# Performance work log

Measured on AMD Instinct MI355X. Metric: run time of the kernel, lower is better.

Reference implementation:

```python
import jax, jax.numpy as jnp
import numpy as np

N = 50000
E = 800000
D_IN = 128
D_OUT = 128


def setup_inputs() -> dict:
    key = jax.random.key(0)
    ks = jax.random.split(key, 12)
    x = jax.random.normal(ks[0], (N, D_IN), dtype=jnp.float32)
    W1 = jax.random.normal(ks[1], (D_IN, D_OUT), dtype=jnp.float32) * (1.0 / np.sqrt(D_IN))
    b1 = jnp.zeros((D_OUT,), dtype=jnp.float32)
    W2 = jax.random.normal(ks[2], (D_IN, D_OUT), dtype=jnp.float32) * (1.0 / np.sqrt(D_IN))
    b2 = jnp.zeros((D_OUT,), dtype=jnp.float32)
    # inverted-dropout masks, p=0.5 -> values in {0, 2}
    def mask(k):
        return jnp.where(jax.random.uniform(k, (N, D_IN)) < 0.5, 0.0, 2.0).astype(jnp.float32)
    mask_pos1 = mask(ks[3])
    mask_neg1 = mask(ks[4])
    mask_pos2 = mask(ks[5])
    mask_neg2 = mask(ks[6])
    edge_index1 = jax.random.randint(ks[7], (2, E), 0, N, dtype=jnp.int32)
    edge_index2 = jax.random.randint(ks[8], (2, E), 0, N, dtype=jnp.int32)
    perm1 = jax.random.permutation(ks[9], N).astype(jnp.int32)
    perm2 = jax.random.permutation(ks[10], N).astype(jnp.int32)
    return dict(x=x, W1=W1, b1=b1, W2=W2, b2=b2,
                mask_pos1=mask_pos1, mask_neg1=mask_neg1,
                mask_pos2=mask_pos2, mask_neg2=mask_neg2,
                edge_index1=edge_index1, edge_index2=edge_index2,
                perm1=perm1, perm2=perm2)


def gcn_conv(x, W, b, edge_index):
    """PyG GCNConv: add self-loops, symmetric normalization, then x@W aggregation + bias."""
    n = x.shape[0]
    xw = x @ W  # [N, D_OUT]
    loops = jnp.arange(n, dtype=edge_index.dtype)
    src = jnp.concatenate([edge_index[0], loops])
    dst = jnp.concatenate([edge_index[1], loops])
    deg = jax.ops.segment_sum(jnp.ones_like(dst, dtype=xw.dtype), dst, num_segments=n)
    dinv = jax.lax.rsqrt(jnp.maximum(deg, 1.0))  # deg >= 1 due to self-loops
    norm = dinv[src] * dinv[dst]                 # [E+N]
    msg = xw[src] * norm[:, None]                # [E+N, D_OUT]
    out = jax.ops.segment_sum(msg, dst, num_segments=n)
    return out + b


def _branch(x, W, b, edge_index, mask_pos, mask_neg, perm):
    pos_h = jax.nn.relu(gcn_conv(x * mask_pos, W, b, edge_index))
    neg_in = (x * mask_neg)[perm]
    neg_h = jax.nn.relu(gcn_conv(neg_in, W, b, edge_index))
    summary = jnp.mean(pos_h, axis=0, keepdims=True)  # [1, D_OUT]
    return pos_h, neg_h, summary


def reference(x, W1, b1, W2, b2, mask_pos1, mask_neg1, mask_pos2, mask_neg2,
              edge_index1, edge_index2, perm1, perm2):
    p1, n1, s1 = _branch(x, W1, b1, edge_index1, mask_pos1, mask_neg1, perm1)
    p2, n2, s2 = _branch(x, W2, b2, edge_index2, mask_pos2, mask_neg2, perm2)
    return (p1, n1, s1, p2, n2, s2)
```

## Files before the change

kernel.cpp:

```cpp
#include <hip/hip_runtime.h>
#include <hip/hip_fp16.h>

#define NN 50000
#define NE 800000
#define D 128
#define GEMM_BLOCKS 3128
#define NBKT 64
#define BW 782
#define BCAP 16384

typedef _Float16 half8_t __attribute__((ext_vector_type(8)));
typedef _Float16 half4_t __attribute__((ext_vector_type(4)));
typedef float f32x4 __attribute__((ext_vector_type(4)));

__global__ void k_init(float* s1, float* s2, int* bcnt,
                       const float* __restrict__ W1, const float* __restrict__ W2,
                       _Float16* wt1, _Float16* wt2) {
    int i = blockIdx.x * 256 + threadIdx.x;
    if (i < D) { s1[i] = 0.f; s2[i] = 0.f; }
    if (i < 2 * NBKT) bcnt[i] = 0;
    int n = i >> 7, k = i & 127;
    wt1[n * 128 + k] = (_Float16)W1[k * 128 + n];
    wt2[n * 128 + k] = (_Float16)W2[k * 128 + n];
}

__global__ void k_bucket(const int* __restrict__ src1, const int* __restrict__ dst1,
                         const int* __restrict__ src2, const int* __restrict__ dst2,
                         int* bcnt,
                         int* bs1, int* bd1, int* bs2, int* bd2) {
    __shared__ int lcnt[128], lpos[128], gbase[128];
    int t = threadIdx.x;
    if (t < 128) { lcnt[t] = 0; lpos[t] = 0; }
    __syncthreads();

    int e0 = blockIdx.x * 256 + t;
    int s1v0=0,d1v0=0,s2v0=0,d2v0=0, s1v1=0,d1v1=0,s2v1=0,d2v1=0;
    int s1v2=0,d1v2=0,s2v2=0,d2v2=0, s1v3=0,d1v3=0,s2v3=0,d2v3=0;
    bool v0 = (e0 + 0 * 262144) < NE;
    bool v1 = (e0 + 1 * 262144) < NE;
    bool v2 = (e0 + 2 * 262144) < NE;
    bool v3 = (e0 + 3 * 262144) < NE;
    if (v0) { int e = e0;             s1v0 = src1[e]; d1v0 = dst1[e]; s2v0 = src2[e]; d2v0 = dst2[e]; }
    if (v1) { int e = e0 + 262144;    s1v1 = src1[e]; d1v1 = dst1[e]; s2v1 = src2[e]; d2v1 = dst2[e]; }
    if (v2) { int e = e0 + 2*262144;  s1v2 = src1[e]; d1v2 = dst1[e]; s2v2 = src2[e]; d2v2 = dst2[e]; }
    if (v3) { int e = e0 + 3*262144;  s1v3 = src1[e]; d1v3 = dst1[e]; s2v3 = src2[e]; d2v3 = dst2[e]; }

    if (v0) { atomicAdd(&lcnt[d1v0 / BW], 1); atomicAdd(&lcnt[NBKT + d2v0 / BW], 1); }
    if (v1) { atomicAdd(&lcnt[d1v1 / BW], 1); atomicAdd(&lcnt[NBKT + d2v1 / BW], 1); }
    if (v2) { atomicAdd(&lcnt[d1v2 / BW], 1); atomicAdd(&lcnt[NBKT + d2v2 / BW], 1); }
    if (v3) { atomicAdd(&lcnt[d1v3 / BW], 1); atomicAdd(&lcnt[NBKT + d2v3 / BW], 1); }
    __syncthreads();
    if (t < 128) gbase[t] = atomicAdd(&bcnt[t], lcnt[t]);
    __syncthreads();

    #define PLACE(sv, dv) { \
        int r = (dv) / BW; \
        int p = gbase[r] + atomicAdd(&lpos[r], 1); \
        if (p < BCAP) { bs1[r * BCAP + p] = (sv); bd1[r * BCAP + p] = (dv); } }
    #define PLACE2(sv, dv) { \
        int r = (dv) / BW; \
        int p = gbase[NBKT + r] + atomicAdd(&lpos[NBKT + r], 1); \
        if (p < BCAP) { bs2[r * BCAP + p] = (sv); bd2[r * BCAP + p] = (dv); } }
    if (v0) { PLACE(s1v0, d1v0); PLACE2(s2v0, d2v0); }
    if (v1) { PLACE(s1v1, d1v1); PLACE2(s2v1, d2v1); }
    if (v2) { PLACE(s1v2, d1v2); PLACE2(s2v2, d2v2); }
    if (v3) { PLACE(s1v3, d1v3); PLACE2(s2v3, d2v3); }
    #undef PLACE
    #undef PLACE2
}

__launch_bounds__(512)
__global__ void k_build(const int* __restrict__ bcnt,
                        const int* __restrict__ bs1, const int* __restrict__ bd1,
                        const int* __restrict__ bs2, const int* __restrict__ bd2,
                        int* rp1, int* rp2, int* col1, int* col2,
                        float* dinv1, float* dinv2) {
    __shared__ int h[1024];
    __shared__ int tsum[512];
    __shared__ int tb[64];
    __shared__ int bbase;
    int t = threadIdx.x;
    int g = blockIdx.x >> 6;
    int f = blockIdx.x & 63;
    const int* bd = (g ? bd2 : bd1) + f * BCAP;
    const int* bs = (g ? bs2 : bs1) + f * BCAP;
    int* rp = g ? rp2 : rp1;
    int* col = g ? col2 : col1;
    float* dinv = g ? dinv2 : dinv1;
    int n = bcnt[g * NBKT + f];
    if (n > BCAP) n = BCAP;

    h[t] = 0; h[t + 512] = 0;
    if (t < NBKT) tb[t] = bcnt[g * NBKT + t];
    __syncthreads();

    for (int i = t; i < n; i += 512) atomicAdd(&h[bd[i] - f * BW], 1);
    __syncthreads();
    if (t == 0) { int b = 0; for (int j = 0; j < f; j++) b += tb[j]; bbase = b; }

    int a0 = h[2 * t], a1 = h[2 * t + 1];
    int s = a0 + a1;
    tsum[t] = s;
    __syncthreads();
    for (int off = 1; off < 512; off <<= 1) {
        int add = (t >= off) ? tsum[t - off] : 0;
        __syncthreads();
        tsum[t] += add;
        __syncthreads();
    }
    int excl = tsum[t] - s + bbase;
    int idx = 2 * t, gd = f * BW + idx;
    int e0 = excl, e1 = excl + a0;
    h[2 * t] = e0; h[2 * t + 1] = e1;
    if (idx < BW && gd < NN)         { rp[gd]     = e0; dinv[gd]     = rsqrtf((float)(a0 + 1)); }
    if (idx + 1 < BW && gd + 1 < NN) { rp[gd + 1] = e1; dinv[gd + 1] = rsqrtf((float)(a1 + 1)); }
    if (f == 63 && t == 0) rp[NN] = NE;
    __syncthreads();

    for (int i = t; i < n; i += 512) {
        int p = atomicAdd(&h[bd[i] - f * BW], 1);
        col[p] = bs[i];
    }
}

__launch_bounds__(256)
__global__ void k_gemm(const _Float16* __restrict__ wt1, const _Float16* __restrict__ wt2,
                       const float* __restrict__ x,
                       const float* __restrict__ mp1, const float* __restrict__ mn1,
                       const float* __restrict__ mp2, const float* __restrict__ mn2,
                       const int* __restrict__ perm1, const int* __restrict__ perm2,
                       const float* __restrict__ dinv1, const float* __restrict__ dinv2,
                       _Float16* xwi1, _Float16* xwi2) {
    __shared__ __align__(16) _Float16 ST[4][16][136];

    int g = blockIdx.x;
    int which = g / 782;
    int bx = g - which * 782;
    const _Float16* wt = (which < 2) ? wt1 : wt2;
    const float* mask = (which == 0) ? mp1 : (which == 1) ? mn1 : (which == 2) ? mp2 : mn2;
    const int* perm = (which == 1) ? perm1 : (which == 3) ? perm2 : nullptr;
    const float* dinv = (which < 2) ? dinv1 : dinv2;
    _Float16* out = ((which < 2) ? xwi1 : xwi2) + ((which & 1) ? 128 : 0);

    int t = threadIdx.x;
    int wave = t >> 6;
    int lane = t & 63;
    int quad = lane >> 4;
    int m = lane & 15;
    int tile = bx * 4 + wave;
    if (tile * 16 >= NN) return;

    int row = tile * 16 + m;
    int grow = perm ? perm[row] : row;
    const float* xrow = x + (long)grow * D;
    const float* mrow = mask + (long)grow * D;

    half8_t a[4];
    #pragma unroll
    for (int kk = 0; kk < 4; kk++) {
        int k0 = kk * 32 + quad * 8;
        float4 xa = *(const float4*)(xrow + k0);
        float4 xb = *(const float4*)(xrow + k0 + 4);
        float4 ma = *(const float4*)(mrow + k0);
        float4 mb = *(const float4*)(mrow + k0 + 4);
        a[kk][0] = (_Float16)(xa.x * ma.x);
        a[kk][1] = (_Float16)(xa.y * ma.y);
        a[kk][2] = (_Float16)(xa.z * ma.z);
        a[kk][3] = (_Float16)(xa.w * ma.w);
        a[kk][4] = (_Float16)(xb.x * mb.x);
        a[kk][5] = (_Float16)(xb.y * mb.y);
        a[kk][6] = (_Float16)(xb.z * mb.z);
        a[kk][7] = (_Float16)(xb.w * mb.w);
    }

    f32x4 accs[8];
    #pragma unroll
    for (int nt = 0; nt < 8; nt++) {
        const _Float16* wrow = wt + (nt * 16 + m) * 128 + quad * 8;
        f32x4 acc = {0.f, 0.f, 0.f, 0.f};
        #pragma unroll
        for (int kk = 0; kk < 4; kk++) {
            half8_t w = *(const half8_t*)(wrow + kk * 32);
            acc = __builtin_amdgcn_mfma_f32_16x16x32_f16(w, a[kk], acc, 0, 0, 0);
        }
        accs[nt] = acc;
    }

    float ds = dinv[tile * 16 + m];
    _Float16* st = &ST[wave][0][0];

    #pragma unroll
    for (int nt = 0; nt < 8; nt++) {
        half4_t h;
        h[0] = (_Float16)(accs[nt][0] * ds);
        h[1] = (_Float16)(accs[nt][1] * ds);
        h[2] = (_Float16)(accs[nt][2] * ds);
        h[3] = (_Float16)(accs[nt][3] * ds);
        *(half4_t*)(st + m * 136 + nt * 16 + quad * 4) = h;
    }
    #pragma unroll
    for (int p = 0; p < 4; p++) {
        int r = lane & 15;
        int cc = (lane >> 4) + p * 4;
        half8_t v = *(const half8_t*)(st + r * 136 + cc * 8);
        *(half8_t*)(out + (long)(tile * 16 + r) * 256 + cc * 8) = v;
    }
}

__launch_bounds__(256)
__global__ void k_agg(const _Float16* __restrict__ xwi1, const _Float16* __restrict__ xwi2,
                      const int* __restrict__ rp1, const int* __restrict__ col1,
                      const float* __restrict__ dinv1,
                      const int* __restrict__ rp2, const int* __restrict__ col2,
                      const float* __restrict__ dinv2,
                      const float* __restrict__ b1, const float* __restrict__ b2,
                      float* out) {
    int g = blockIdx.y;
    const _Float16* xwi = g ? xwi2 : xwi1;
    const int* rp = g ? rp2 : rp1;
    const int* col = g ? col2 : col1;
    const float* dinv = g ? dinv2 : dinv1;
    const float* bias = g ? b2 : b1;
    float* pos_out = out + (g ? 12800128L : 0L);
    float* neg_out = out + (g ? 19200128L : 6400000L);

    int t = threadIdx.x;
    int wave = t >> 6, lane = t & 63;
    int i = blockIdx.x * 4 + wave;
    if (i >= NN) return;
    int j4 = lane * 4;

    half4_t sv = *(const half4_t*)(xwi + (long)i * 256 + j4);
    float a0 = (float)sv[0], a1 = (float)sv[1], a2 = (float)sv[2], a3 = (float)sv[3];
    int e0 = rp[i], e1 = rp[i + 1];
    int e = e0;
    for (; e + 8 <= e1; e += 8) {
        int s0 = col[e + 0], s1 = col[e + 1], s2 = col[e + 2], s3 = col[e + 3];
        int s4 = col[e + 4], s5 = col[e + 5], s6 = col[e + 6], s7 = col[e + 7];
        half4_t v0 = *(const half4_t*)(xwi + (long)s0 * 256 + j4);
        half4_t v1 = *(const half4_t*)(xwi + (long)s1 * 256 + j4);
        half4_t v2 = *(const half4_t*)(xwi + (long)s2 * 256 + j4);
        half4_t v3 = *(const half4_t*)(xwi + (long)s3 * 256 + j4);
        half4_t v4 = *(const half4_t*)(xwi + (long)s4 * 256 + j4);
        half4_t v5 = *(const half4_t*)(xwi + (long)s5 * 256 + j4);
        half4_t v6 = *(const half4_t*)(xwi + (long)s6 * 256 + j4);
        half4_t v7 = *(const half4_t*)(xwi + (long)s7 * 256 + j4);
        a0 += (float)v0[0] + (float)v1[0] + (float)v2[0] + (float)v3[0]
            + (float)v4[0] + (float)v5[0] + (float)v6[0] + (float)v7[0];
        a1 += (float)v0[1] + (float)v1[1] + (float)v2[1] + (float)v3[1]
            + (float)v4[1] + (float)v5[1] + (float)v6[1] + (float)v7[1];
        a2 += (float)v0[2] + (float)v1[2] + (float)v2[2] + (float)v3[2]
            + (float)v4[2] + (float)v5[2] + (float)v6[2] + (float)v7[2];
        a3 += (float)v0[3] + (float)v1[3] + (float)v2[3] + (float)v3[3]
            + (float)v4[3] + (float)v5[3] + (float)v6[3] + (float)v7[3];
    }
    for (; e + 4 <= e1; e += 4) {
        int s0 = col[e + 0], s1 = col[e + 1], s2 = col[e + 2], s3 = col[e + 3];
        half4_t v0 = *(const half4_t*)(xwi + (long)s0 * 256 + j4);
        half4_t v1 = *(const half4_t*)(xwi + (long)s1 * 256 + j4);
        half4_t v2 = *(const half4_t*)(xwi + (long)s2 * 256 + j4);
        half4_t v3 = *(const half4_t*)(xwi + (long)s3 * 256 + j4);
        a0 += (float)v0[0] + (float)v1[0] + (float)v2[0] + (float)v3[0];
        a1 += (float)v0[1] + (float)v1[1] + (float)v2[1] + (float)v3[1];
        a2 += (float)v0[2] + (float)v1[2] + (float)v2[2] + (float)v3[2];
        a3 += (float)v0[3] + (float)v1[3] + (float)v2[3] + (float)v3[3];
    }
    for (; e < e1; e++) {
        int s = col[e];
        half4_t v = *(const half4_t*)(xwi + (long)s * 256 + j4);
        a0 += (float)v[0]; a1 += (float)v[1]; a2 += (float)v[2]; a3 += (float)v[3];
    }
    float di = dinv[i];
    int jj = (lane < 32) ? j4 : (j4 - 128);
    const f32x4* bp = (const f32x4*)(bias + jj);
    f32x4 bv = *bp;
    f32x4 o;
    o[0] = fmaxf(0.f, di * a0 + bv[0]);
    o[1] = fmaxf(0.f, di * a1 + bv[1]);
    o[2] = fmaxf(0.f, di * a2 + bv[2]);
    o[3] = fmaxf(0.f, di * a3 + bv[3]);
    float* dst = ((lane < 32) ? pos_out : neg_out) + (long)i * D + jj;
    __builtin_nontemporal_store(o, (f32x4*)dst);
}

__launch_bounds__(256)
__global__ void k_sum(const float* __restrict__ pos1, const float* __restrict__ pos2,
                      float* s1, float* s2) {
    int g = blockIdx.y;
    const float* pos = g ? pos2 : pos1;
    float* s = g ? s2 : s1;
    int t = threadIdx.x;
    int rg = t >> 5;
    int j = (t & 31) * 4;
    float4 acc = {0.f, 0.f, 0.f, 0.f};
    for (int i = blockIdx.x * 8 + rg; i < NN; i += gridDim.x * 8) {
        float4 v = *(const float4*)(pos + (long)i * D + j);
        acc.x += v.x; acc.y += v.y; acc.z += v.z; acc.w += v.w;
    }
    __shared__ float sm[8][128];
    sm[rg][j + 0] = acc.x;
    sm[rg][j + 1] = acc.y;
    sm[rg][j + 2] = acc.z;
    sm[rg][j + 3] = acc.w;
    __syncthreads();
    if (t < 128) {
        float v = 0.f;
        for (int r = 0; r < 8; r++) v += sm[r][t];
        atomicAdd(&s[t], v * (1.0f / NN));
    }
}

extern "C" void kernel_launch(void* const* d_in, const int* in_sizes, int n_in,
                              void* d_out, int out_size, void* d_ws, size_t ws_size,
                              hipStream_t stream) {
    const float* x   = (const float*)d_in[0];
    const float* W1  = (const float*)d_in[1];
    const float* b1  = (const float*)d_in[2];
    const float* W2  = (const float*)d_in[3];
    const float* b2  = (const float*)d_in[4];
    const float* mp1 = (const float*)d_in[5];
    const float* mn1 = (const float*)d_in[6];
    const float* mp2 = (const float*)d_in[7];
    const float* mn2 = (const float*)d_in[8];
    const int* e1 = (const int*)d_in[9];
    const int* e2 = (const int*)d_in[10];
    const int* perm1 = (const int*)d_in[11];
    const int* perm2 = (const int*)d_in[12];
    const int* src1 = e1;       const int* dst1 = e1 + NE;
    const int* src2 = e2;       const int* dst2 = e2 + NE;
    float* out = (float*)d_out;

    char* w = (char*)d_ws;
    _Float16* xwi1 = (_Float16*)w; w += (size_t)NN * 256 * 2;
    _Float16* xwi2 = (_Float16*)w; w += (size_t)NN * 256 * 2;
    int* rp1 = (int*)w;   w += (size_t)(NN + 4) * 4;
    int* rp2 = (int*)w;   w += (size_t)(NN + 4) * 4;
    int* col1 = (int*)w;  w += (size_t)NE * 4;
    int* col2 = (int*)w;  w += (size_t)NE * 4;
    float* dinv1 = (float*)w; w += (size_t)NN * 4;
    float* dinv2 = (float*)w; w += (size_t)NN * 4;
    int* bcnt  = (int*)w; w += (size_t)128 * 4;
    int* bs1 = (int*)w;   w += (size_t)NBKT * BCAP * 4;
    int* bd1 = (int*)w;   w += (size_t)NBKT * BCAP * 4;
    int* bs2 = (int*)w;   w += (size_t)NBKT * BCAP * 4;
    int* bd2 = (int*)w;   w += (size_t)NBKT * BCAP * 4;
    _Float16* wt1 = (_Float16*)w; w += (size_t)D * D * 2;
    _Float16* wt2 = (_Float16*)w; w += (size_t)D * D * 2;

    float* s1 = out + 12800000L;
    float* s2 = out + 25600128L;
    const float* pos1 = out;
    const float* pos2 = out + 12800128L;

    k_init<<<dim3(64), 256, 0, stream>>>(s1, s2, bcnt, W1, W2, wt1, wt2);
    k_bucket<<<dim3(1024), 256, 0, stream>>>(src1, dst1, src2, dst2, bcnt,
                                             bs1, bd1, bs2, bd2);
    k_build<<<dim3(128), 512, 0, stream>>>(bcnt, bs1, bd1, bs2, bd2,
                                           rp1, rp2, col1, col2, dinv1, dinv2);
    k_gemm<<<dim3(GEMM_BLOCKS), 256, 0, stream>>>(wt1, wt2,
        x, mp1, mn1, mp2, mn2, perm1, perm2, dinv1, dinv2, xwi1, xwi2);
    k_agg<<<dim3(12500, 2), 256, 0, stream>>>(xwi1, xwi2,
                                              rp1, col1, dinv1, rp2, col2, dinv2,
                                              b1, b2, out);
    k_sum<<<dim3(128, 2), 256, 0, stream>>>(pos1, pos2, s1, s2);
}
```

Before: 465.6 us.

## Fuse summary mean into aggregation, invert permutation for coalesced GEMM reads

The negative-branch GEMM now reads x and mask rows sequentially and scatters each output row through an inverse permutation built in k_init, instead of gathering permuted input rows. The column-mean summary is accumulated inside the aggregation kernel through shared-memory atomics and 64 global slots per branch, which removes the separate pass that re-read the positive outputs. Bucket source and destination pairs are packed into int2, and mask loads are marked nontemporal. The cost is extra atomics in k_agg, a scattered write of the fp16 intermediate, and two small extra kernels' worth of work.

After: 453.3 us. -2.7%, faster.

```diff
diff --git a/kernel.cpp b/kernel.cpp
--- a/kernel.cpp
+++ b/kernel.cpp
@@ -13,21 +13,25 @@
 typedef _Float16 half4_t __attribute__((ext_vector_type(4)));
 typedef float f32x4 __attribute__((ext_vector_type(4)));
 
-__global__ void k_init(float* s1, float* s2, int* bcnt,
+__global__ void k_init(float* ssl, int* bcnt,
                        const float* __restrict__ W1, const float* __restrict__ W2,
-                       _Float16* wt1, _Float16* wt2) {
+                       _Float16* wt1, _Float16* wt2,
+                       const int* __restrict__ perm1, const int* __restrict__ perm2,
+                       int* pinv1, int* pinv2) {
     int i = blockIdx.x * 256 + threadIdx.x;
-    if (i < D) { s1[i] = 0.f; s2[i] = 0.f; }
+    if (i < NN) { pinv1[perm1[i]] = i; pinv2[perm2[i]] = i; }
     if (i < 2 * NBKT) bcnt[i] = 0;
-    int n = i >> 7, k = i & 127;
-    wt1[n * 128 + k] = (_Float16)W1[k * 128 + n];
-    wt2[n * 128 + k] = (_Float16)W2[k * 128 + n];
+    if (i < 16384) {
+        ssl[i] = 0.f;
+        int n = i >> 7, k = i & 127;
+        wt1[n * 128 + k] = (_Float16)W1[k * 128 + n];
+        wt2[n * 128 + k] = (_Float16)W2[k * 128 + n];
+    }
 }
 
 __global__ void k_bucket(const int* __restrict__ src1, const int* __restrict__ dst1,
                          const int* __restrict__ src2, const int* __restrict__ dst2,
-                         int* bcnt,
-                         int* bs1, int* bd1, int* bs2, int* bd2) {
+                         int* bcnt, int2* bsd1, int2* bsd2) {
     __shared__ int lcnt[128], lpos[128], gbase[128];
     int t = threadIdx.x;
     if (t < 128) { lcnt[t] = 0; lpos[t] = 0; }
@@ -56,11 +60,11 @@
     #define PLACE(sv, dv) { \
         int r = (dv) / BW; \
         int p = gbase[r] + atomicAdd(&lpos[r], 1); \
-        if (p < BCAP) { bs1[r * BCAP + p] = (sv); bd1[r * BCAP + p] = (dv); } }
+        if (p < BCAP) bsd1[r * BCAP + p] = make_int2((sv), (dv)); }
     #define PLACE2(sv, dv) { \
         int r = (dv) / BW; \
         int p = gbase[NBKT + r] + atomicAdd(&lpos[NBKT + r], 1); \
-        if (p < BCAP) { bs2[r * BCAP + p] = (sv); bd2[r * BCAP + p] = (dv); } }
+        if (p < BCAP) bsd2[r * BCAP + p] = make_int2((sv), (dv)); }
     if (v0) { PLACE(s1v0, d1v0); PLACE2(s2v0, d2v0); }
     if (v1) { PLACE(s1v1, d1v1); PLACE2(s2v1, d2v1); }
     if (v2) { PLACE(s1v2, d1v2); PLACE2(s2v2, d2v2); }
@@ -71,8 +75,7 @@
 
 __launch_bounds__(512)
 __global__ void k_build(const int* __restrict__ bcnt,
-                        const int* __restrict__ bs1, const int* __restrict__ bd1,
-                        const int* __restrict__ bs2, const int* __restrict__ bd2,
+                        const int2* __restrict__ bsd1, const int2* __restrict__ bsd2,
                         int* rp1, int* rp2, int* col1, int* col2,
                         float* dinv1, float* dinv2) {
     __shared__ int h[1024];
@@ -82,8 +85,7 @@
     int t = threadIdx.x;
     int g = blockIdx.x >> 6;
     int f = blockIdx.x & 63;
-    const int* bd = (g ? bd2 : bd1) + f * BCAP;
-    const int* bs = (g ? bs2 : bs1) + f * BCAP;
+    const int2* bsd = (g ? bsd2 : bsd1) + f * BCAP;
     int* rp = g ? rp2 : rp1;
     int* col = g ? col2 : col1;
     float* dinv = g ? dinv2 : dinv1;
@@ -94,7 +96,7 @@
     if (t < NBKT) tb[t] = bcnt[g * NBKT + t];
     __syncthreads();
 
-    for (int i = t; i < n; i += 512) atomicAdd(&h[bd[i] - f * BW], 1);
+    for (int i = t; i < n; i += 512) atomicAdd(&h[bsd[i].y - f * BW], 1);
     __syncthreads();
     if (t == 0) { int b = 0; for (int j = 0; j < f; j++) b += tb[j]; bbase = b; }
 
@@ -118,8 +120,9 @@
     __syncthreads();
 
     for (int i = t; i < n; i += 512) {
-        int p = atomicAdd(&h[bd[i] - f * BW], 1);
-        col[p] = bs[i];
+        int2 e = bsd[i];
+        int p = atomicAdd(&h[e.y - f * BW], 1);
+        col[p] = e.x;
     }
 }
 
@@ -128,7 +131,7 @@
                        const float* __restrict__ x,
                        const float* __restrict__ mp1, const float* __restrict__ mn1,
                        const float* __restrict__ mp2, const float* __restrict__ mn2,
-                       const int* __restrict__ perm1, const int* __restrict__ perm2,
+                       const int* __restrict__ pinv1, const int* __restrict__ pinv2,
                        const float* __restrict__ dinv1, const float* __restrict__ dinv2,
                        _Float16* xwi1, _Float16* xwi2) {
     __shared__ __align__(16) _Float16 ST[4][16][136];
@@ -138,7 +141,7 @@
     int bx = g - which * 782;
     const _Float16* wt = (which < 2) ? wt1 : wt2;
     const float* mask = (which == 0) ? mp1 : (which == 1) ? mn1 : (which == 2) ? mp2 : mn2;
-    const int* perm = (which == 1) ? perm1 : (which == 3) ? perm2 : nullptr;
+    const int* pinv = (which == 1) ? pinv1 : (which == 3) ? pinv2 : nullptr;
     const float* dinv = (which < 2) ? dinv1 : dinv2;
     _Float16* out = ((which < 2) ? xwi1 : xwi2) + ((which & 1) ? 128 : 0);
 
@@ -151,26 +154,25 @@
     if (tile * 16 >= NN) return;
 
     int row = tile * 16 + m;
-    int grow = perm ? perm[row] : row;
-    const float* xrow = x + (long)grow * D;
-    const float* mrow = mask + (long)grow * D;
+    const float* xrow = x + (long)row * D;
+    const float* mrow = mask + (long)row * D;
 
     half8_t a[4];
     #pragma unroll
     for (int kk = 0; kk < 4; kk++) {
         int k0 = kk * 32 + quad * 8;
-        float4 xa = *(const float4*)(xrow + k0);
-        float4 xb = *(const float4*)(xrow + k0 + 4);
-        float4 ma = *(const float4*)(mrow + k0);
-        float4 mb = *(const float4*)(mrow + k0 + 4);
-        a[kk][0] = (_Float16)(xa.x * ma.x);
-        a[kk][1] = (_Float16)(xa.y * ma.y);
-        a[kk][2] = (_Float16)(xa.z * ma.z);
-        a[kk][3] = (_Float16)(xa.w * ma.w);
-        a[kk][4] = (_Float16)(xb.x * mb.x);
-        a[kk][5] = (_Float16)(xb.y * mb.y);
-        a[kk][6] = (_Float16)(xb.z * mb.z);
-        a[kk][7] = (_Float16)(xb.w * mb.w);
+        f32x4 xa = *(const f32x4*)(xrow + k0);
+        f32x4 xb = *(const f32x4*)(xrow + k0 + 4);
+        f32x4 ma = __builtin_nontemporal_load((const f32x4*)(mrow + k0));
+        f32x4 mb = __builtin_nontemporal_load((const f32x4*)(mrow + k0 + 4));
+        a[kk][0] = (_Float16)(xa[0] * ma[0]);
+        a[kk][1] = (_Float16)(xa[1] * ma[1]);
+        a[kk][2] = (_Float16)(xa[2] * ma[2]);
+        a[kk][3] = (_Float16)(xa[3] * ma[3]);
+        a[kk][4] = (_Float16)(xb[0] * mb[0]);
+        a[kk][5] = (_Float16)(xb[1] * mb[1]);
+        a[kk][6] = (_Float16)(xb[2] * mb[2]);
+        a[kk][7] = (_Float16)(xb[3] * mb[3]);
     }
 
     f32x4 accs[8];
@@ -186,7 +188,8 @@
         accs[nt] = acc;
     }
 
-    float ds = dinv[tile * 16 + m];
+    int orow = pinv ? pinv[row] : row;
+    float ds = dinv[orow];
     _Float16* st = &ST[wave][0][0];
 
     #pragma unroll
@@ -200,10 +203,9 @@
     }
     #pragma unroll
     for (int p = 0; p < 4; p++) {
-        int r = lane & 15;
         int cc = (lane >> 4) + p * 4;
-        half8_t v = *(const half8_t*)(st + r * 136 + cc * 8);
-        *(half8_t*)(out + (long)(tile * 16 + r) * 256 + cc * 8) = v;
+        half8_t v = *(const half8_t*)(st + m * 136 + cc * 8);
+        *(half8_t*)(out + (long)orow * 256 + cc * 8) = v;
     }
 }
 
@@ -214,7 +216,8 @@
                       const int* __restrict__ rp2, const int* __restrict__ col2,
                       const float* __restrict__ dinv2,
                       const float* __restrict__ b1, const float* __restrict__ b2,
-                      float* out) {
+                      float* out, float* ssl) {
+    __shared__ float ssum[128];
     int g = blockIdx.y;
     const _Float16* xwi = g ? xwi2 : xwi1;
     const int* rp = g ? rp2 : rp1;
@@ -225,9 +228,11 @@
     float* neg_out = out + (g ? 19200128L : 6400000L);
 
     int t = threadIdx.x;
+    if (t < 128) ssum[t] = 0.f;
+    __syncthreads();
+
     int wave = t >> 6, lane = t & 63;
     int i = blockIdx.x * 4 + wave;
-    if (i >= NN) return;
     int j4 = lane * 4;
 
     half4_t sv = *(const half4_t*)(xwi + (long)i * 256 + j4);
@@ -281,33 +286,25 @@
     o[3] = fmaxf(0.f, di * a3 + bv[3]);
     float* dst = ((lane < 32) ? pos_out : neg_out) + (long)i * D + jj;
     __builtin_nontemporal_store(o, (f32x4*)dst);
-}
-
-__launch_bounds__(256)
-__global__ void k_sum(const float* __restrict__ pos1, const float* __restrict__ pos2,
-                      float* s1, float* s2) {
+
+    if (lane < 32) {
+        atomicAdd(&ssum[j4 + 0], o[0]);
+        atomicAdd(&ssum[j4 + 1], o[1]);
+        atomicAdd(&ssum[j4 + 2], o[2]);
+        atomicAdd(&ssum[j4 + 3], o[3]);
+    }
+    __syncthreads();
+    if (t < 128) atomicAdd(&ssl[(long)g * 8192 + (blockIdx.x & 63) * 128 + t], ssum[t]);
+}
+
+__global__ void k_sumf(const float* __restrict__ ssl, float* s1, float* s2) {
     int g = blockIdx.y;
-    const float* pos = g ? pos2 : pos1;
-    float* s = g ? s2 : s1;
-    int t = threadIdx.x;
-    int rg = t >> 5;
-    int j = (t & 31) * 4;
-    float4 acc = {0.f, 0.f, 0.f, 0.f};
-    for (int i = blockIdx.x * 8 + rg; i < NN; i += gridDim.x * 8) {
-        float4 v = *(const float4*)(pos + (long)i * D + j);
-        acc.x += v.x; acc.y += v.y; acc.z += v.z; acc.w += v.w;
-    }
-    __shared__ float sm[8][128];
-    sm[rg][j + 0] = acc.x;
-    sm[rg][j + 1] = acc.y;
-    sm[rg][j + 2] = acc.z;
-    sm[rg][j + 3] = acc.w;
-    __syncthreads();
-    if (t < 128) {
-        float v = 0.f;
-        for (int r = 0; r < 8; r++) v += sm[r][t];
-        atomicAdd(&s[t], v * (1.0f / NN));
-    }
+    int t = threadIdx.x;
+    const float* p = ssl + (long)g * 8192;
+    float v = 0.f;
+    #pragma unroll
+    for (int sl = 0; sl < 64; sl++) v += p[sl * 128 + t];
+    (g ? s2 : s1)[t] = v * (1.0f / NN);
 }
 
 extern "C" void kernel_launch(void* const* d_in, const int* in_sizes, int n_in,
@@ -340,27 +337,26 @@
     float* dinv1 = (float*)w; w += (size_t)NN * 4;
     float* dinv2 = (float*)w; w += (size_t)NN * 4;
     int* bcnt  = (int*)w; w += (size_t)128 * 4;
-    int* bs1 = (int*)w;   w += (size_t)NBKT * BCAP * 4;
-    int* bd1 = (int*)w;   w += (size_t)NBKT * BCAP * 4;
-    int* bs2 = (int*)w;   w += (size_t)NBKT * BCAP * 4;
-    int* bd2 = (int*)w;   w += (size_t)NBKT * BCAP * 4;
+    int2* bsd1 = (int2*)w; w += (size_t)NBKT * BCAP * 8;
+    int2* bsd2 = (int2*)w; w += (size_t)NBKT * BCAP * 8;
     _Float16* wt1 = (_Float16*)w; w += (size_t)D * D * 2;
     _Float16* wt2 = (_Float16*)w; w += (size_t)D * D * 2;
+    int* pinv1 = (int*)w; w += (size_t)NN * 4;
+    int* pinv2 = (int*)w; w += (size_t)NN * 4;
+    float* ssl = (float*)w; w += (size_t)2 * 64 * 128 * 4;
 
     float* s1 = out + 12800000L;
     float* s2 = out + 25600128L;
-    const float* pos1 = out;
-    const float* pos2 = out + 12800128L;
-
-    k_init<<<dim3(64), 256, 0, stream>>>(s1, s2, bcnt, W1, W2, wt1, wt2);
-    k_bucket<<<dim3(1024), 256, 0, stream>>>(src1, dst1, src2, dst2, bcnt,
-                                             bs1, bd1, bs2, bd2);
-    k_build<<<dim3(128), 512, 0, stream>>>(bcnt, bs1, bd1, bs2, bd2,
+
+    k_init<<<dim3(196), 256, 0, stream>>>(ssl, bcnt, W1, W2, wt1, wt2,
+                                          perm1, perm2, pinv1, pinv2);
+    k_bucket<<<dim3(1024), 256, 0, stream>>>(src1, dst1, src2, dst2, bcnt, bsd1, bsd2);
+    k_build<<<dim3(128), 512, 0, stream>>>(bcnt, bsd1, bsd2,
                                            rp1, rp2, col1, col2, dinv1, dinv2);
     k_gemm<<<dim3(GEMM_BLOCKS), 256, 0, stream>>>(wt1, wt2,
-        x, mp1, mn1, mp2, mn2, perm1, perm2, dinv1, dinv2, xwi1, xwi2);
+        x, mp1, mn1, mp2, mn2, pinv1, pinv2, dinv1, dinv2, xwi1, xwi2);
     k_agg<<<dim3(12500, 2), 256, 0, stream>>>(xwi1, xwi2,
                                               rp1, col1, dinv1, rp2, col2, dinv2,
-                                              b1, b2, out);
-    k_sum<<<dim3(128, 2), 256, 0, stream>>>(pos1, pos2, s1, s2);
-}
+                                              b1, b2, out, ssl);
+    k_sumf<<<dim3(1, 2), 128, 0, stream>>>(ssl, s1, s2);
+}
```
